# Optimization experiments

Measured on AMD Instinct MI355X. Metric: run time of the kernel, lower is better.

The kernel has to match this reference:

```python
import jax, jax.numpy as jnp
import numpy as np
from jax import lax
import math

POOL = 7
SPATIAL_SCALE = 0.125
SCORE_THRESH = 0.05
NMS_THRESH = 0.5
DET_PER_IMG = 100
NUM_CLASSES = 81
NUM_STAGES = 3
FEAT_CH = 256
CLIP_VAL = math.log(1000.0 / 16)
STDS = ((0.1, 0.1, 0.2, 0.2), (0.05, 0.05, 0.1, 0.1), (0.033, 0.033, 0.067, 0.067))


def setup_inputs() -> dict:
    key = jax.random.key(0)
    ks = jax.random.split(key, 12)
    B, N, img = 2, 512, 512
    features = jax.random.normal(ks[0], (B, FEAT_CH, 64, 64), jnp.float32)
    cx = jax.random.uniform(ks[1], (B, N)) * img
    cy = jax.random.uniform(ks[2], (B, N)) * img
    w = 16.0 + jax.random.uniform(ks[3], (B, N)) * 240.0
    h = 16.0 + jax.random.uniform(ks[4], (B, N)) * 240.0
    proposals = jnp.stack([
        jnp.clip(cx - 0.5 * w, 0.0, img), jnp.clip(cy - 0.5 * h, 0.0, img),
        jnp.clip(cx + 0.5 * w, 0.0, img), jnp.clip(cy + 0.5 * h, 0.0, img)], axis=-1)
    in_dim = FEAT_CH * POOL * POOL
    sc = 0.02
    return {
        'features': features,
        'proposals': proposals,
        'fc1_w': jax.random.normal(ks[5], (NUM_STAGES, in_dim, 1024), jnp.float32) * sc,
        'fc1_b': jnp.zeros((NUM_STAGES, 1024), jnp.float32),
        'fc2_w': jax.random.normal(ks[6], (NUM_STAGES, 1024, 1024), jnp.float32) * sc,
        'fc2_b': jnp.zeros((NUM_STAGES, 1024), jnp.float32),
        'cls_w': jax.random.normal(ks[7], (NUM_STAGES, 1024, NUM_CLASSES), jnp.float32) * sc,
        'cls_b': jnp.zeros((NUM_STAGES, NUM_CLASSES), jnp.float32),
        'bbox_w': jax.random.normal(ks[8], (NUM_STAGES, 1024, 4), jnp.float32) * sc,
        'bbox_b': jnp.zeros((NUM_STAGES, 4), jnp.float32),
        'image_size': 512,
    }


def _bilinear(feat, gx, gy):
    # feat [C,H,W]; gx,gy [N,P,P] float coords
    C, H, W = feat.shape
    x = jnp.clip(gx, 0.0, W - 1.0)
    y = jnp.clip(gy, 0.0, H - 1.0)
    x0f, y0f = jnp.floor(x), jnp.floor(y)
    x0 = x0f.astype(jnp.int32)
    y0 = y0f.astype(jnp.int32)
    x1 = jnp.minimum(x0 + 1, W - 1)
    y1 = jnp.minimum(y0 + 1, H - 1)
    dx = (x - x0f)[None]
    dy = (y - y0f)[None]
    v = (feat[:, y0, x0] * (1 - dy) * (1 - dx) + feat[:, y0, x1] * (1 - dy) * dx
         + feat[:, y1, x0] * dy * (1 - dx) + feat[:, y1, x1] * dy * dx)
    return v  # [C,N,P,P]


def roi_align(feat, boxes):
    # feat [C,H,W], boxes [N,4] in feature-map coords
    x1, y1, x2, y2 = boxes[:, 0], boxes[:, 1], boxes[:, 2], boxes[:, 3]
    bw = jnp.maximum(x2 - x1, 1.0) / POOL
    bh = jnp.maximum(y2 - y1, 1.0) / POOL
    c = jnp.arange(POOL, dtype=boxes.dtype) + 0.5
    xs = x1[:, None] + c * bw[:, None]  # [N,P]
    ys = y1[:, None] + c * bh[:, None]
    N = boxes.shape[0]
    gx = jnp.broadcast_to(xs[:, None, :], (N, POOL, POOL))
    gy = jnp.broadcast_to(ys[:, :, None], (N, POOL, POOL))
    return jnp.transpose(_bilinear(feat, gx, gy), (1, 0, 2, 3))  # [N,C,P,P]


def decode_boxes(proposals, deltas, stds):
    px1, py1, px2, py2 = proposals[:, 0], proposals[:, 1], proposals[:, 2], proposals[:, 3]
    pw = jnp.maximum(px2 - px1, 1e-6)
    ph = jnp.maximum(py2 - py1, 1e-6)
    pcx = px1 + 0.5 * pw
    pcy = py1 + 0.5 * ph
    wx, wy, ww, wh = stds
    dx = deltas[:, 0] * wx
    dy = deltas[:, 1] * wy
    dw = jnp.minimum(deltas[:, 2] * ww, CLIP_VAL)
    dh = jnp.minimum(deltas[:, 3] * wh, CLIP_VAL)
    cx = dx * pw + pcx
    cy = dy * ph + pcy
    w = jnp.exp(dw) * pw
    h = jnp.exp(dh) * ph
    return jnp.stack([cx - 0.5 * w, cy - 0.5 * h, cx + 0.5 * w, cy + 0.5 * h], axis=1)


def clip_boxes(b, img):
    return jnp.stack([jnp.clip(b[:, 0], 0.0, img), jnp.clip(b[:, 1], 0.0, img),
                      jnp.clip(b[:, 2], 0.0, img), jnp.clip(b[:, 3], 0.0, img)], axis=1)


def nms_per_image(boxes, probs, img):
    # boxes [N,4], probs [N,C]
    N, C = probs.shape
    Cm = C - 1  # skip background class 0
    labels = jnp.broadcast_to(jnp.arange(1, C, dtype=jnp.int32), (N, Cm)).reshape(-1)
    b = jnp.broadcast_to(boxes[:, None, :], (N, Cm, 4)).reshape(-1, 4)
    s = probs[:, 1:].reshape(-1)
    ws = b[:, 2] - b[:, 0]
    hs = b[:, 3] - b[:, 1]
    valid = (s > SCORE_THRESH) & (ws >= 1.0) & (hs >= 1.0)
    s = jnp.where(valid, s, -1.0)
    # class-offset trick == batched_nms
    ob = b + (labels.astype(b.dtype) * (img + 2.0))[:, None]
    area = jnp.maximum(ob[:, 2] - ob[:, 0], 0.0) * jnp.maximum(ob[:, 3] - ob[:, 1], 0.0)

    def step(s_live, _):
        i = jnp.argmax(s_live)
        si = s_live[i]
        bi = ob[i]
        ix1 = jnp.maximum(bi[0], ob[:, 0])
        iy1 = jnp.maximum(bi[1], ob[:, 1])
        ix2 = jnp.minimum(bi[2], ob[:, 2])
        iy2 = jnp.minimum(bi[3], ob[:, 3])
        inter = jnp.maximum(ix2 - ix1, 0.0) * jnp.maximum(iy2 - iy1, 0.0)
        iou = inter / (area[i] + area - inter + 1e-9)
        s_live = jnp.where(iou > NMS_THRESH, -1.0, s_live)
        s_live = s_live.at[i].set(-1.0)
        return s_live, (i, si)

    _, (idx, sel_s) = lax.scan(step, s, None, length=DET_PER_IMG)
    flag = sel_s > 0.0
    out_boxes = jnp.where(flag[:, None], b[idx], 0.0)
    out_scores = jnp.where(flag, sel_s, 0.0)
    out_labels = jnp.where(flag, labels[idx], 0)
    return out_boxes, out_scores, out_labels


def reference(features, proposals, fc1_w, fc1_b, fc2_w, fc2_b, cls_w, cls_b, bbox_w, bbox_b, image_size):
    B, Cf, H, W = features.shape
    N = proposals.shape[1]
    img = float(image_size)
    cur = proposals  # [B,N,4]
    logits = None
    for st in range(NUM_STAGES):
        pooled = jax.vmap(lambda f, bx: roi_align(f, bx * SPATIAL_SCALE))(features, cur)  # [B,N,C,P,P]
        x = pooled.reshape(B * N, -1)
        x = jax.nn.relu(x @ fc1_w[st] + fc1_b[st])
        x = jax.nn.relu(x @ fc2_w[st] + fc2_b[st])
        logits = x @ cls_w[st] + cls_b[st]  # [B*N, C]
        deltas = x @ bbox_w[st] + bbox_b[st]  # [B*N, 4]
        dec = clip_boxes(decode_boxes(cur.reshape(-1, 4), deltas, STDS[st]), img)
        cur = dec.reshape(B, N, 4)
    probs = jax.nn.softmax(logits.reshape(B, N, -1), axis=-1)
    boxes, scores, labels = jax.vmap(lambda bb, pp: nms_per_image(bb, pp, img))(cur, probs)
    return boxes, scores, labels
```

## Files before the change

### kernel.cpp

```cpp
#include <hip/hip_runtime.h>
#include <math.h>

#define NPROP 512
#define NB 2
#define NROWS (NB*NPROP)
#define FCH 256
#define FH 64
#define FW 64
#define INDIM (FCH*7*7)
#define HID 1024
#define NCLS 81
#define CAND_PER_IMG (NPROP*(NCLS-1))
#define CLIPV 4.1351666f

typedef _Float16 f16x8 __attribute__((ext_vector_type(8)));
typedef float f32x4 __attribute__((ext_vector_type(4)));
typedef unsigned int u32;
typedef unsigned long long u64;

__device__ __forceinline__ void gload16(const void* g, void* l) {
    __builtin_amdgcn_global_load_lds((const __attribute__((address_space(1))) u32*)g,
                                     (__attribute__((address_space(3))) u32*)l, 16, 0, 0);
}


#define XHI_OFF    0ull
#define XLO_OFF    25690112ull
#define WT1HI_OFF  51380224ull
#define WT1LO_OFF  77070336ull
#define WT2HI_OFF  102760448ull
#define WT2LO_OFF  104857600ull
#define H1HI_OFF   106954752ull
#define H1LO_OFF   109051904ull
#define H2_OFF     111149056ull
#define CWT_OFF    115343360ull
#define BWT_OFF    116338688ull
#define PROBS_OFF  116387840ull
#define CUR_OFF    116719616ull
#define CNT_OFF    116736000ull
#define CCS_OFF    116737024ull
#define CCOB_OFF   117064704ull
#define CCAR_OFF   118375424ull
#define CCBX_OFF   118703104ull
#define CCIX_OFF   120013824ull
#define SVS_OFF    120341504ull
#define SVB_OFF    120423424ull
#define SVI_OFF    120751104ull
#define SVC_OFF    120833024ull
#define PART_OFF   121489408ull

__global__ void init_kernel(int* ccnt) {
    if (threadIdx.x < 160) ccnt[threadIdx.x] = 0;
}

__global__ __launch_bounds__(256) void roi_align_kernel(
    const float* __restrict__ feat, const float* __restrict__ boxes,
    _Float16* __restrict__ Xhi, _Float16* __restrict__ Xlo)
{
    int r = blockIdx.x;
    int b = r >> 9;
    const float* f = feat + (size_t)b * (FCH*FH*FW);
    __shared__ float sb[4];
    __shared__ int   sx0[49], sx1[49], sy0[49], sy1[49];
    __shared__ float sw00[49], sw01[49], sw10[49], sw11[49];
    int tid = threadIdx.x;
    if (tid == 0) {
        float x1 = boxes[r*4+0]*0.125f, y1 = boxes[r*4+1]*0.125f;
        float x2 = boxes[r*4+2]*0.125f, y2 = boxes[r*4+3]*0.125f;
        sb[0] = x1; sb[1] = y1;
        sb[2] = fmaxf(x2-x1, 1.0f) / 7.0f;
        sb[3] = fmaxf(y2-y1, 1.0f) / 7.0f;
    }
    __syncthreads();
    if (tid < 49) {
        int py = tid / 7, px = tid - py*7;
        float gx = sb[0] + ((float)px + 0.5f)*sb[2];
        float gy = sb[1] + ((float)py + 0.5f)*sb[3];
        gx = fminf(fmaxf(gx, 0.0f), 63.0f);
        gy = fminf(fmaxf(gy, 0.0f), 63.0f);
        float x0f = floorf(gx), y0f = floorf(gy);
        int x0 = (int)x0f, y0 = (int)y0f;
        sx0[tid] = x0; sy0[tid] = y0;
        sx1[tid] = min(x0+1, 63); sy1[tid] = min(y0+1, 63);
        float dx = gx - x0f, dy = gy - y0f;
        sw00[tid] = (1.0f-dy)*(1.0f-dx);
        sw01[tid] = (1.0f-dy)*dx;
        sw10[tid] = dy*(1.0f-dx);
        sw11[tid] = dy*dx;
    }
    __syncthreads();
    for (int i = tid; i < INDIM; i += 256) {
        int c = i / 49;
        int p = i - c*49;
        const float* fc = f + c*(FH*FW);
        int r0 = sy0[p]*FW, r1 = sy1[p]*FW;
        float v = fc[r0 + sx0[p]]*sw00[p] + fc[r0 + sx1[p]]*sw01[p]
                + fc[r1 + sx0[p]]*sw10[p] + fc[r1 + sx1[p]]*sw11[p];
        float vs = v * 32.0f;
        _Float16 h = (_Float16)vs;
        size_t idx = ((size_t)(i >> 3) << 13) + ((size_t)r << 3) + (i & 7);
        Xhi[idx] = h;
        Xlo[idx] = (_Float16)(vs - (float)h);
    }
}

__global__ __launch_bounds__(256) void trans_limb(
    const float* __restrict__ in, _Float16* __restrict__ hi, _Float16* __restrict__ lo,
    int K, int N, float scale)
{
    __shared__ float t[32][33];
    int tx = threadIdx.x & 31, ty = threadIdx.x >> 5;
    int n0 = blockIdx.x << 5, k0 = blockIdx.y << 5;
#pragma unroll
    for (int r = 0; r < 4; ++r)
        t[ty + 8*r][tx] = in[(size_t)(k0 + ty + 8*r)*N + n0 + tx];
    __syncthreads();
#pragma unroll
    for (int r = 0; r < 4; ++r) {
        int n = n0 + ty + 8*r, k = k0 + tx;
        float v = t[tx][ty + 8*r] * scale;
        _Float16 h = (_Float16)v;
        size_t idx = ((size_t)(k >> 3)*N << 3) + ((size_t)n << 3) + (k & 7);
        hi[idx] = h;
        lo[idx] = (_Float16)(v - (float)h);
    }
}

__global__ __launch_bounds__(256) void trans_naive(
    const float* __restrict__ in, float* __restrict__ out, int K, int N, int batch)
{
    int idx = blockIdx.x*256 + threadIdx.x;
    int per = K*N;
    if (idx >= per*batch) return;
    int b = idx / per;
    int rem = idx - b*per;
    int n = rem / K, k = rem - n*K;
    out[idx] = in[(size_t)b*per + (size_t)k*N + n];
}

__global__ __launch_bounds__(512, 2) void mfma_gemm_limb256(
    const _Float16* __restrict__ Ahi, const _Float16* __restrict__ Alo,
    const _Float16* __restrict__ Bhi, const _Float16* __restrict__ Blo,
    float* __restrict__ part, int base, int extra)
{
    extern __shared__ __align__(16) char ldsraw[];
    const int tid = threadIdx.x;
    const int lane = tid & 63;
    const int w = tid >> 6;
    const int wm = w >> 2, wn = w & 3;
    const int kg = lane >> 4, lr = lane & 15;
    const int bid = blockIdx.x;
    const int z = bid & 15;
    const int tile = bid >> 4;
    const int bx = tile & 3, by = tile >> 2;
    const int row0 = by << 8, col0 = bx << 8;
    const int zsteps = base + (z < extra ? 1 : 0);
    const int o0 = ((z*base + (z < extra ? z : extra)) * 32) >> 3;

    const int sp = w >> 1;
    const int sbase = (w & 1) * 8;
    const _Float16* pl = (sp == 0) ? Ahi : (sp == 1) ? Alo : (sp == 2) ? Bhi : Blo;
    const int rc0 = (sp < 2) ? row0 : col0;
    const _Float16* sG = pl + ((size_t)(rc0 + lane) << 3);

    f32x4 acc[8][4];
#pragma unroll
    for (int i = 0; i < 8; ++i)
#pragma unroll
        for (int j = 0; j < 4; ++j) acc[i][j] = (f32x4){0.f, 0.f, 0.f, 0.f};

    auto STAGE = [&](int bufoff, int koct) {
#pragma unroll
        for (int j = 0; j < 8; ++j) {
            int sub = sbase + j;
            int ks = sub >> 2, rblk = sub & 3;
            const void* g = (const void*)(sG + ((size_t)(o0 + koct + ks) << 13)
                                             + ((size_t)rblk << 9));
            void* l = (void*)(ldsraw + bufoff + sp*16384 + ks*4096 + rblk*1024);
            gload16(g, l);
        }
    };

    STAGE(0, 0);
    if (zsteps > 1) STAGE(65536, 4);

    for (int t = 0; t < zsteps; ++t) {
        if (t + 1 < zsteps) asm volatile("s_waitcnt vmcnt(8)" ::: "memory");
        else                asm volatile("s_waitcnt vmcnt(0)" ::: "memory");
        __builtin_amdgcn_s_barrier();
        asm volatile("" ::: "memory");
        const char* Lb = ldsraw + ((t & 1) ? 65536 : 0);
        f16x8 Bh[4], Bl[4];
#pragma unroll
        for (int ni = 0; ni < 4; ++ni) {
            int s = (kg*256 + wn*64 + ni*16 + lr) * 16;
            Bh[ni] = *(const f16x8*)(Lb + 2*16384 + s);
            Bl[ni] = *(const f16x8*)(Lb + 3*16384 + s);
        }
#pragma unroll
        for (int mi = 0; mi < 8; ++mi) {
            int s = (kg*256 + wm*128 + mi*16 + lr) * 16;
            f16x8 ah = *(const f16x8*)(Lb + s);
            f16x8 al = *(const f16x8*)(Lb + 16384 + s);
#pragma unroll
            for (int ni = 0; ni < 4; ++ni) {
                acc[mi][ni] = __builtin_amdgcn_mfma_f32_16x16x32_f16(ah, Bh[ni], acc[mi][ni], 0, 0, 0);
                acc[mi][ni] = __builtin_amdgcn_mfma_f32_16x16x32_f16(ah, Bl[ni], acc[mi][ni], 0, 0, 0);
                acc[mi][ni] = __builtin_amdgcn_mfma_f32_16x16x32_f16(al, Bh[ni], acc[mi][ni], 0, 0, 0);
            }
        }
        asm volatile("" ::: "memory");
        __builtin_amdgcn_s_barrier();
        asm volatile("" ::: "memory");
        if (t + 2 < zsteps) STAGE((t & 1) ? 65536 : 0, (t+2)*4);
    }

    float* cb = part + ((size_t)z << 20)
              + (size_t)row0*HID + col0 + wn*64 + lr;
#pragma unroll
    for (int mi = 0; mi < 8; ++mi) {
#pragma unroll
        for (int j = 0; j < 4; ++j) {
            int row = wm*128 + mi*16 + kg*4 + j;
            float* pr = cb + (size_t)row*HID;
            pr[0]  = acc[mi][0][j];
            pr[16] = acc[mi][1][j];
            pr[32] = acc[mi][2][j];
            pr[48] = acc[mi][3][j];
        }
    }
}

__global__ __launch_bounds__(256) void mfma_gemm_limb(
    const _Float16* __restrict__ Ahi, const _Float16* __restrict__ Alo,
    const _Float16* __restrict__ Bhi, const _Float16* __restrict__ Blo,
    float* __restrict__ part, int base, int extra, int lognz)
{
    __shared__ __align__(16) _Float16 lds[2][4][512][8];
    const int tid = threadIdx.x;
    const int lane = tid & 63;
    const int w = tid >> 6, wm = w >> 1, wn = w & 1;
    const int kg = lane >> 4, lr = lane & 15;
    const int bid = blockIdx.x;
    const int nzm = (1 << lognz) - 1;
    const int z = bid & nzm;
    const int bx = (bid >> lognz) & 7;
    const int by = bid >> (lognz + 3);
    const int row0 = by << 7, col0 = bx << 7;
    const int zsteps = base + (z < extra ? 1 : 0);
    const int o0 = ((z*base + (z < extra ? z : extra)) * 32) >> 3;
    const int r_ = tid & 127;
    const int ks1 = tid >> 7;
    const int wb = tid & 192;

    const _Float16* srcA0 = Ahi + ((size_t)(row0 + r_) << 3);
    const _Float16* srcA1 = Alo + ((size_t)(row0 + r_) << 3);
    const _Float16* srcB0 = Bhi + ((size_t)(col0 + r_) << 3);
    const _Float16* srcB1 = Blo + ((size_t)(col0 + r_) << 3);

    f32x4 acc[4][4];
#pragma unroll
    for (int i = 0; i < 4; ++i)
#pragma unroll
        for (int j = 0; j < 4; ++j) acc[i][j] = (f32x4){0.f, 0.f, 0.f, 0.f};

#define STAGE(bf, oct) do { \
    _Float16* Lb = &lds[bf][0][0][0]; \
    gload16(srcA0 + ((size_t)(o0+(oct)+ks1  ) << 13), (void*)(Lb + (0*512 +       wb)*8)); \
    gload16(srcA0 + ((size_t)(o0+(oct)+ks1+2) << 13), (void*)(Lb + (0*512 + 256 + wb)*8)); \
    gload16(srcA1 + ((size_t)(o0+(oct)+ks1  ) << 13), (void*)(Lb + (1*512 +       wb)*8)); \
    gload16(srcA1 + ((size_t)(o0+(oct)+ks1+2) << 13), (void*)(Lb + (1*512 + 256 + wb)*8)); \
    gload16(srcB0 + ((size_t)(o0+(oct)+ks1  ) << 13), (void*)(Lb + (2*512 +       wb)*8)); \
    gload16(srcB0 + ((size_t)(o0+(oct)+ks1+2) << 13), (void*)(Lb + (2*512 + 256 + wb)*8)); \
    gload16(srcB1 + ((size_t)(o0+(oct)+ks1  ) << 13), (void*)(Lb + (3*512 +       wb)*8)); \
    gload16(srcB1 + ((size_t)(o0+(oct)+ks1+2) << 13), (void*)(Lb + (3*512 + 256 + wb)*8)); \
} while (0)

    STAGE(0, 0);
    if (1 < zsteps) STAGE(1, 4);
    for (int t = 0; t < zsteps; ++t) {
        if (t + 1 < zsteps) asm volatile("s_waitcnt vmcnt(8)" ::: "memory");
        else                asm volatile("s_waitcnt vmcnt(0)" ::: "memory");
        __builtin_amdgcn_s_barrier();
        const _Float16* Lr = &lds[t & 1][0][0][0];
        f16x8 Ah[4], Al[4], Bh[4], Bl[4];
#pragma unroll
        for (int mi = 0; mi < 4; ++mi) {
            int s = kg*128 + wm*64 + mi*16 + lr;
            Ah[mi] = *(const f16x8*)(Lr + (0*512 + s)*8);
            Al[mi] = *(const f16x8*)(Lr + (1*512 + s)*8);
        }
#pragma unroll
        for (int ni = 0; ni < 4; ++ni) {
            int s = kg*128 + wn*64 + ni*16 + lr;
            Bh[ni] = *(const f16x8*)(Lr + (2*512 + s)*8);
            Bl[ni] = *(const f16x8*)(Lr + (3*512 + s)*8);
        }
        asm volatile("s_waitcnt lgkmcnt(0)" ::: "memory");
        __builtin_amdgcn_sched_barrier(0);
        __builtin_amdgcn_s_barrier();
        if (t + 2 < zsteps) STAGE(t & 1, (t+2)*4);
#pragma unroll
        for (int mi = 0; mi < 4; ++mi)
#pragma unroll
            for (int ni = 0; ni < 4; ++ni) {
                acc[mi][ni] = __builtin_amdgcn_mfma_f32_16x16x32_f16(Ah[mi], Bh[ni], acc[mi][ni], 0, 0, 0);
                acc[mi][ni] = __builtin_amdgcn_mfma_f32_16x16x32_f16(Ah[mi], Bl[ni], acc[mi][ni], 0, 0, 0);
                acc[mi][ni] = __builtin_amdgcn_mfma_f32_16x16x32_f16(Al[mi], Bh[ni], acc[mi][ni], 0, 0, 0);
            }
    }
#undef STAGE

    float* cb = part + ((size_t)z << 20)
              + (size_t)row0*HID + col0 + wn*64 + lr;
#pragma unroll
    for (int mi = 0; mi < 4; ++mi) {
#pragma unroll
        for (int j = 0; j < 4; ++j) {
            int row = wm*64 + mi*16 + kg*4 + j;
            float* pr = cb + (size_t)row*HID;
            pr[0]  = acc[mi][0][j];
            pr[16] = acc[mi][1][j];
            pr[32] = acc[mi][2][j];
            pr[48] = acc[mi][3][j];
        }
    }
}

__global__ __launch_bounds__(256) void reduce_bias_relu(
    const float* __restrict__ part, const float* __restrict__ bias,
    float* __restrict__ out32, _Float16* __restrict__ outhi, _Float16* __restrict__ outlo,
    int nsplit, int mode)
{
    int gid = blockIdx.x*256 + threadIdx.x;
    float s = 0.f;
    for (int p = 0; p < nsplit; ++p) s += part[((size_t)p << 20) + gid];
    s = s * (1.0f/2048.0f) + bias[gid & (HID-1)];
    s = fmaxf(s, 0.f);
    if (mode == 0) {
        out32[gid] = s;
    } else {
        float vs = s * 32.0f;
        _Float16 h = (_Float16)vs;
        int row = gid >> 10, col = gid & 1023;
        size_t idx = ((size_t)(col >> 3) << 13) + ((size_t)row << 3) + (col & 7);
        outhi[idx] = h;
        outlo[idx] = (_Float16)(vs - (float)h);
    }
}

__global__ __launch_bounds__(512) void heads_kernel(
    const float* __restrict__ X, const float* __restrict__ cwT, const float* __restrict__ cb,
    const float* __restrict__ bwT, const float* __restrict__ bbb,
    float* __restrict__ cur, float* __restrict__ probs,
    const int* __restrict__ img_sz, int stage, int write_probs)
{
    __shared__ float xs[4][1024];
    __shared__ float lg[4][96];
    int tid = threadIdx.x;
    int lr = tid >> 7;
    int j  = tid & 127;
    int row0 = blockIdx.x * 4;
    for (int i = tid; i < 4096; i += 512)
        xs[i >> 10][i & 1023] = X[(size_t)(row0 + (i >> 10))*1024 + (i & 1023)];
    __syncthreads();
    int row = row0 + lr;
    if (j < 85) {
        const float* wrow = (j < 81) ? (cwT + (size_t)j*HID) : (bwT + (size_t)(j-81)*HID);
        float acc = (j < 81) ? cb[j] : bbb[j-81];
        const float4* w4 = (const float4*)wrow;
#pragma unroll 4
        for (int k4 = 0; k4 < 256; ++k4) {
            float4 wv = w4[k4];
            const float* xr = &xs[lr][k4*4];
            acc = fmaf(xr[0], wv.x, acc);
            acc = fmaf(xr[1], wv.y, acc);
            acc = fmaf(xr[2], wv.z, acc);
            acc = fmaf(xr[3], wv.w, acc);
        }
        lg[lr][j] = acc;
    }
    __syncthreads();
    if (j == 0) {
        float img = (float)(*img_sz);
        float px1 = cur[row*4+0], py1 = cur[row*4+1];
        float px2 = cur[row*4+2], py2 = cur[row*4+3];
        float pw = fmaxf(px2-px1, 1e-6f), ph = fmaxf(py2-py1, 1e-6f);
        float pcx = px1 + 0.5f*pw, pcy = py1 + 0.5f*ph;
        float wx, wy, ww, wh;
        if (stage == 0)      { wx=0.1f;   wy=0.1f;   ww=0.2f;   wh=0.2f;   }
        else if (stage == 1) { wx=0.05f;  wy=0.05f;  ww=0.1f;   wh=0.1f;   }
        else                 { wx=0.033f; wy=0.033f; ww=0.067f; wh=0.067f; }
        float dx = lg[lr][81]*wx, dy = lg[lr][82]*wy;
        float dw = fminf(lg[lr][83]*ww, CLIPV);
        float dh = fminf(lg[lr][84]*wh, CLIPV);
        float cx = dx*pw + pcx, cy = dy*ph + pcy;
        float w = expf(dw)*pw, h = expf(dh)*ph;
        cur[row*4+0] = fminf(fmaxf(cx - 0.5f*w, 0.f), img);
        cur[row*4+1] = fminf(fmaxf(cy - 0.5f*h, 0.f), img);
        cur[row*4+2] = fminf(fmaxf(cx + 0.5f*w, 0.f), img);
        cur[row*4+3] = fminf(fmaxf(cy + 0.5f*h, 0.f), img);
    }
    if (write_probs) {
        if (j == 1) {
            float m = lg[lr][0];
            for (int c2 = 1; c2 < 81; ++c2) m = fmaxf(m, lg[lr][c2]);
            float s = 0.f;
            for (int c2 = 0; c2 < 81; ++c2) s += expf(lg[lr][c2] - m);
            lg[lr][88] = m; lg[lr][89] = s;
        }
        __syncthreads();
        if (j < 81)
            probs[(size_t)row*81 + j] = expf(lg[lr][j] - lg[lr][88]) / lg[lr][89];
    }
}

__global__ __launch_bounds__(256) void compact_class(
    const float* __restrict__ probs, const float* __restrict__ cur,
    const int* __restrict__ img_sz, int* __restrict__ ccnt,
    float* __restrict__ ccs, float4* __restrict__ ccob, float* __restrict__ ccar,
    float4* __restrict__ ccbx, int* __restrict__ ccix)
{
    int gid = blockIdx.x*256 + threadIdx.x;
    if (gid >= NB*CAND_PER_IMG) return;
    int b = gid / CAND_PER_IMG;
    int rem = gid - b*CAND_PER_IMG;
    int n = rem / 80;
    int cm = rem - n*80;
    int label = cm + 1;
    int r = b*NPROP + n;
    float s = probs[(size_t)r*81 + label];
    float b0 = cur[r*4+0], b1 = cur[r*4+1], b2 = cur[r*4+2], b3 = cur[r*4+3];
    if (s > 0.05f && (b2 - b0) >= 1.0f && (b3 - b1) >= 1.0f) {
        int cls = b*80 + cm;
        int pos = atomicAdd(&ccnt[cls], 1);
        int base = cls*512 + pos;
        float img = (float)(*img_sz);
        float t = (float)label * (img + 2.0f);
        float o0 = b0+t, o1 = b1+t, o2 = b2+t, o3 = b3+t;
        ccs[base] = s;
        ccob[base] = make_float4(o0, o1, o2, o3);
        ccar[base] = fmaxf(o2-o0, 0.f) * fmaxf(o3-o1, 0.f);
        ccbx[base] = make_float4(b0, b1, b2, b3);
        ccix[base] = rem;
    }
}

__global__ __launch_bounds__(64) void class_nms(
    const int* __restrict__ ccnt, const float* __restrict__ ccs,
    const float4* __restrict__ ccob, const float* __restrict__ ccar,
    const float4* __restrict__ ccbx, const int* __restrict__ ccix,
    float* __restrict__ svs, float4* __restrict__ svb, int* __restrict__ svi,
    int* __restrict__ svc)
{
    int cls = blockIdx.x;
    int Nc = ccnt[cls];
    int base = cls*512;
    int lane = threadIdx.x;
    __shared__ float sel[5];
    float s[8]; float4 ob[8]; float a[8]; int ix[8];
    int cntl = 0;
    for (int j = lane; j < Nc; j += 64) {
        s[cntl] = ccs[base+j]; ob[cntl] = ccob[base+j];
        a[cntl] = ccar[base+j]; ix[cntl] = ccix[base+j];
        ++cntl;
    }
    int svn = 0;
    int rounds = (Nc < 100) ? Nc : 100;
    for (int it = 0; it < rounds; ++it) {
        float bs = -1.f; int bi = 0x7fffffff;
        for (int q = 0; q < cntl; ++q)
            if (s[q] > bs || (s[q] == bs && ix[q] < bi)) { bs = s[q]; bi = ix[q]; }
        for (int off = 32; off > 0; off >>= 1) {
            float os = __shfl_xor(bs, off);
            int oi = __shfl_xor(bi, off);
            if (os > bs || (os == bs && oi < bi)) { bs = os; bi = oi; }
        }
        if (bs <= 0.f) break;
        for (int q = 0; q < cntl; ++q) {
            if (s[q] == bs && ix[q] == bi) {
                sel[0] = ob[q].x; sel[1] = ob[q].y; sel[2] = ob[q].z; sel[3] = ob[q].w;
                sel[4] = a[q];
                int slot = cls*128 + svn;
                svs[slot] = bs;
                svb[slot] = ccbx[base + lane + q*64];
                svi[slot] = bi;
                s[q] = -1.f;
            }
        }
        __syncthreads();
        float bi0 = sel[0], bi1 = sel[1], bi2 = sel[2], bi3 = sel[3], ai = sel[4];
        for (int q = 0; q < cntl; ++q) {
            if (s[q] > 0.f) {
                float ix1 = fmaxf(bi0, ob[q].x), iy1 = fmaxf(bi1, ob[q].y);
                float ix2 = fminf(bi2, ob[q].z), iy2 = fminf(bi3, ob[q].w);
                float inter = fmaxf(ix2-ix1, 0.f) * fmaxf(iy2-iy1, 0.f);
                float iou = inter / (ai + a[q] - inter + 1e-9f);
                if (iou > 0.5f) s[q] = -1.f;
            }
        }
        ++svn;
        __syncthreads();
    }
    if (lane == 0) svc[cls] = svn;
}

__global__ __launch_bounds__(256) void merge_topk(
    const float* __restrict__ svs, const float4* __restrict__ svb,
    const int* __restrict__ svi, const int* __restrict__ svc,
    float* __restrict__ out)
{
    extern __shared__ char smem[];
    u64* keys = (u64*)smem;
    u32* pay  = (u32*)(smem + 65536);
    __shared__ int off[81];
    __shared__ int n2s;
    int b = blockIdx.x, tid = threadIdx.x;
    if (tid == 0) {
        int run = 0;
        for (int c = 0; c < 80; ++c) { off[c] = run; run += svc[b*80 + c]; }
        off[80] = run;
        int n2 = 256;
        while (n2 < run) n2 <<= 1;
        n2s = n2;
    }
    __syncthreads();
    int Ns = off[80], n2 = n2s;
    for (int c = 0; c < 80; ++c) {
        int n = off[c+1] - off[c];
        int srcb = (b*80 + c)*128;
        for (int k = tid; k < n; k += 256) {
            int src = srcb + k;
            keys[off[c] + k] = ((u64)__float_as_uint(svs[src]) << 32)
                             | (u64)(0xFFFFFFFFu - (u32)svi[src]);
            pay[off[c] + k] = src;
        }
    }
    for (int i = Ns + tid; i < n2; i += 256) { keys[i] = 0; pay[i] = 0; }
    __syncthreads();
    for (int k = 2; k <= n2; k <<= 1) {
        for (int j = k >> 1; j > 0; j >>= 1) {
            for (int i = tid; i < n2; i += 256) {
                int l = i ^ j;
                if (l > i) {
                    u64 a = keys[i], bb = keys[l];
                    bool dir = ((i & k) == 0);
                    if ((a < bb) == dir) {
                        keys[i] = bb; keys[l] = a;
                        u32 p = pay[i]; pay[i] = pay[l]; pay[l] = p;
                    }
                }
            }
            __syncthreads();
        }
    }
    if (tid < 100) {
        u64 kk = keys[tid];
        if (kk != 0) {
            u32 ci = 0xFFFFFFFFu - (u32)(kk & 0xFFFFFFFFull);
            float4 bx = svb[pay[tid]];
            out[b*400 + tid*4 + 0] = bx.x;
            out[b*400 + tid*4 + 1] = bx.y;
            out[b*400 + tid*4 + 2] = bx.z;
            out[b*400 + tid*4 + 3] = bx.w;
            out[800  + b*100 + tid] = __uint_as_float((u32)(kk >> 32));
            out[1000 + b*100 + tid] = (float)((ci % 80) + 1);
        } else {
            out[b*400 + tid*4 + 0] = 0.f; out[b*400 + tid*4 + 1] = 0.f;
            out[b*400 + tid*4 + 2] = 0.f; out[b*400 + tid*4 + 3] = 0.f;
            out[800  + b*100 + tid] = 0.f;
            out[1000 + b*100 + tid] = 0.f;
        }
    }
}

extern "C" void kernel_launch(void* const* d_in, const int* in_sizes, int n_in,
                              void* d_out, int out_size, void* d_ws, size_t ws_size,
                              hipStream_t stream)
{
    const float* features  = (const float*)d_in[0];
    const float* proposals = (const float*)d_in[1];
    const float* fc1_w = (const float*)d_in[2];
    const float* fc1_b = (const float*)d_in[3];
    const float* fc2_w = (const float*)d_in[4];
    const float* fc2_b = (const float*)d_in[5];
    const float* cls_w = (const float*)d_in[6];
    const float* cls_b = (const float*)d_in[7];
    const float* bbox_w = (const float*)d_in[8];
    const float* bbox_b = (const float*)d_in[9];
    const int* img_sz = (const int*)d_in[10];
    float* out = (float*)d_out;
    char* ws = (char*)d_ws;
    _Float16* xhi   = (_Float16*)(ws + XHI_OFF);
    _Float16* xlo   = (_Float16*)(ws + XLO_OFF);
    _Float16* wt1hi = (_Float16*)(ws + WT1HI_OFF);
    _Float16* wt1lo = (_Float16*)(ws + WT1LO_OFF);
    _Float16* wt2hi = (_Float16*)(ws + WT2HI_OFF);
    _Float16* wt2lo = (_Float16*)(ws + WT2LO_OFF);
    _Float16* h1hi  = (_Float16*)(ws + H1HI_OFF);
    _Float16* h1lo  = (_Float16*)(ws + H1LO_OFF);
    float*  h2     = (float*) (ws + H2_OFF);
    float*  cwT    = (float*) (ws + CWT_OFF);
    float*  bwT    = (float*) (ws + BWT_OFF);
    float*  probs  = (float*) (ws + PROBS_OFF);
    float*  cur    = (float*) (ws + CUR_OFF);
    int*    ccnt   = (int*)   (ws + CNT_OFF);
    float*  ccs    = (float*) (ws + CCS_OFF);
    float4* ccob   = (float4*)(ws + CCOB_OFF);
    float*  ccar   = (float*) (ws + CCAR_OFF);
    float4* ccbx   = (float4*)(ws + CCBX_OFF);
    int*    ccix   = (int*)   (ws + CCIX_OFF);
    float*  svs    = (float*) (ws + SVS_OFF);
    float4* svb    = (float4*)(ws + SVB_OFF);
    int*    svi    = (int*)   (ws + SVI_OFF);
    int*    svc    = (int*)   (ws + SVC_OFF);
    float*  part   = (float*) (ws + PART_OFF);

    init_kernel<<<1, 256, 0, stream>>>(ccnt);
    hipMemcpyAsync(cur, proposals, (size_t)NROWS*4*sizeof(float),
                   hipMemcpyDeviceToDevice, stream);
    trans_naive<<<(3*NCLS*HID + 255)/256, 256, 0, stream>>>(cls_w, cwT, HID, NCLS, 3);
    trans_naive<<<(3*4*HID + 255)/256, 256, 0, stream>>>(bbox_w, bwT, HID, 4, 3);

    for (int st = 0; st < 3; ++st) {
        roi_align_kernel<<<NROWS, 256, 0, stream>>>(features, cur, xhi, xlo);
        trans_limb<<<dim3(HID/32, INDIM/32), 256, 0, stream>>>(
            fc1_w + (size_t)st*INDIM*HID, wt1hi, wt1lo, INDIM, HID, 64.0f);
        mfma_gemm_limb256<<<256, 512, 131072, stream>>>(
            xhi, xlo, wt1hi, wt1lo, part, 24, 8);
        reduce_bias_relu<<<(NROWS*HID)/256, 256, 0, stream>>>(
            part, fc1_b + st*HID, nullptr, h1hi, h1lo, 16, 1);
        trans_limb<<<dim3(HID/32, HID/32), 256, 0, stream>>>(
            fc2_w + (size_t)st*HID*HID, wt2hi, wt2lo, HID, HID, 64.0f);
        mfma_gemm_limb<<<512, 256, 0, stream>>>(
            h1hi, h1lo, wt2hi, wt2lo, part, 4, 0, 3);
        reduce_bias_relu<<<(NROWS*HID)/256, 256, 0, stream>>>(
            part, fc2_b + st*HID, h2, nullptr, nullptr, 8, 0);
        heads_kernel<<<NROWS/4, 512, 0, stream>>>(
            h2, cwT + (size_t)st*NCLS*HID, cls_b + st*NCLS,
            bwT + (size_t)st*4*HID, bbox_b + st*4,
            cur, probs, img_sz, st, st == 2 ? 1 : 0);
    }
    compact_class<<<(NB*CAND_PER_IMG)/256, 256, 0, stream>>>(
        probs, cur, img_sz, ccnt, ccs, ccob, ccar, ccbx, ccix);
    class_nms<<<160, 64, 0, stream>>>(
        ccnt, ccs, ccob, ccar, ccbx, ccix, svs, svb, svi, svc);
    merge_topk<<<NB, 256, 98304, stream>>>(
        svs, svb, svi, svc, out);
}
```

Baseline: 781.2 us.

## Stage ROI-align and weight-limb outputs in shared memory for vectorized 16-byte stores

ROI-align now handles four ROIs per block, one wavefront each. It precomputes the flat bilinear indices and weights, stages the fp16 hi/lo results in shared memory by channel chunk, and writes them out as 16-byte vectors in the k-octet-major layout instead of scattered 2-byte stores. trans_limb likewise packs eight k values per thread and issues f16x8 stores. The GEMM loop adds an explicit LDS waitcnt and a sched_barrier before the s_barrier, presumably for correctness or scheduling. The cost is more LDS use and fewer, larger ROI blocks.

```diff
diff --git a/kernel.cpp b/kernel.cpp
--- a/kernel.cpp
+++ b/kernel.cpp
@@ -12,6 +12,7 @@
 #define NCLS 81
 #define CAND_PER_IMG (NPROP*(NCLS-1))
 #define CLIPV 4.1351666f
+#define RCHUNK 1792
 
 typedef _Float16 f16x8 __attribute__((ext_vector_type(8)));
 typedef float f32x4 __attribute__((ext_vector_type(4)));
@@ -57,50 +58,63 @@
     const float* __restrict__ feat, const float* __restrict__ boxes,
     _Float16* __restrict__ Xhi, _Float16* __restrict__ Xlo)
 {
-    int r = blockIdx.x;
-    int b = r >> 9;
+    __shared__ __align__(16) _Float16 bufh[4][1800], bufl[4][1800];
+    __shared__ int   sidx[4][4][49];
+    __shared__ float swt[4][4][49];
+    const int tid = threadIdx.x;
+    const int w = tid >> 6, lane = tid & 63;
+    const int r0 = blockIdx.x << 2;
+    const int r = r0 + w;
+    const int b = r >> 9;
     const float* f = feat + (size_t)b * (FCH*FH*FW);
-    __shared__ float sb[4];
-    __shared__ int   sx0[49], sx1[49], sy0[49], sy1[49];
-    __shared__ float sw00[49], sw01[49], sw10[49], sw11[49];
-    int tid = threadIdx.x;
-    if (tid == 0) {
+
+    if (lane < 49) {
         float x1 = boxes[r*4+0]*0.125f, y1 = boxes[r*4+1]*0.125f;
         float x2 = boxes[r*4+2]*0.125f, y2 = boxes[r*4+3]*0.125f;
-        sb[0] = x1; sb[1] = y1;
-        sb[2] = fmaxf(x2-x1, 1.0f) / 7.0f;
-        sb[3] = fmaxf(y2-y1, 1.0f) / 7.0f;
-    }
-    __syncthreads();
-    if (tid < 49) {
-        int py = tid / 7, px = tid - py*7;
-        float gx = sb[0] + ((float)px + 0.5f)*sb[2];
-        float gy = sb[1] + ((float)py + 0.5f)*sb[3];
+        float bw = fmaxf(x2-x1, 1.0f) / 7.0f;
+        float bh = fmaxf(y2-y1, 1.0f) / 7.0f;
+        int py = lane / 7, px = lane - py*7;
+        float gx = x1 + ((float)px + 0.5f)*bw;
+        float gy = y1 + ((float)py + 0.5f)*bh;
         gx = fminf(fmaxf(gx, 0.0f), 63.0f);
         gy = fminf(fmaxf(gy, 0.0f), 63.0f);
         float x0f = floorf(gx), y0f = floorf(gy);
         int x0 = (int)x0f, y0 = (int)y0f;
-        sx0[tid] = x0; sy0[tid] = y0;
-        sx1[tid] = min(x0+1, 63); sy1[tid] = min(y0+1, 63);
+        int x1c = min(x0+1, 63), y1c = min(y0+1, 63);
         float dx = gx - x0f, dy = gy - y0f;
-        sw00[tid] = (1.0f-dy)*(1.0f-dx);
-        sw01[tid] = (1.0f-dy)*dx;
-        sw10[tid] = dy*(1.0f-dx);
-        sw11[tid] = dy*dx;
+        sidx[w][0][lane] = y0*FW + x0;
+        sidx[w][1][lane] = y0*FW + x1c;
+        sidx[w][2][lane] = y1c*FW + x0;
+        sidx[w][3][lane] = y1c*FW + x1c;
+        swt[w][0][lane] = (1.0f-dy)*(1.0f-dx);
+        swt[w][1][lane] = (1.0f-dy)*dx;
+        swt[w][2][lane] = dy*(1.0f-dx);
+        swt[w][3][lane] = dy*dx;
     }
     __syncthreads();
-    for (int i = tid; i < INDIM; i += 256) {
-        int c = i / 49;
-        int p = i - c*49;
-        const float* fc = f + c*(FH*FW);
-        int r0 = sy0[p]*FW, r1 = sy1[p]*FW;
-        float v = fc[r0 + sx0[p]]*sw00[p] + fc[r0 + sx1[p]]*sw01[p]
-                + fc[r1 + sx0[p]]*sw10[p] + fc[r1 + sx1[p]]*sw11[p];
-        float vs = v * 32.0f;
-        _Float16 h = (_Float16)vs;
-        size_t idx = ((size_t)(i >> 3) << 13) + ((size_t)r << 3) + (i & 7);
-        Xhi[idx] = h;
-        Xlo[idx] = (_Float16)(vs - (float)h);
+    for (int ch = 0; ch < 7; ++ch) {
+        for (int i2 = lane; i2 < RCHUNK; i2 += 64) {
+            int i = ch*RCHUNK + i2;
+            int c = i / 49;
+            int p = i - c*49;
+            const float* fc = f + c*(FH*FW);
+            float v = fc[sidx[w][0][p]]*swt[w][0][p] + fc[sidx[w][1][p]]*swt[w][1][p]
+                    + fc[sidx[w][2][p]]*swt[w][2][p] + fc[sidx[w][3][p]]*swt[w][3][p];
+            float vs = v * 32.0f;
+            _Float16 h = (_Float16)vs;
+            bufh[w][i2] = h;
+            bufl[w][i2] = (_Float16)(vs - (float)h);
+        }
+        __syncthreads();
+        for (int q = tid; q < 224*4; q += 256) {
+            int oct = q >> 2, p = q & 3;
+            f16x8 hv = *(const f16x8*)&bufh[p][oct*8];
+            f16x8 lv = *(const f16x8*)&bufl[p][oct*8];
+            size_t idx = ((size_t)(ch*224 + oct) << 13) + ((size_t)(r0 + p) << 3);
+            *(f16x8*)(Xhi + idx) = hv;
+            *(f16x8*)(Xlo + idx) = lv;
+        }
+        __syncthreads();
     }
 }
 
@@ -115,14 +129,19 @@
     for (int r = 0; r < 4; ++r)
         t[ty + 8*r][tx] = in[(size_t)(k0 + ty + 8*r)*N + n0 + tx];
     __syncthreads();
-#pragma unroll
-    for (int r = 0; r < 4; ++r) {
-        int n = n0 + ty + 8*r, k = k0 + tx;
-        float v = t[tx][ty + 8*r] * scale;
-        _Float16 h = (_Float16)v;
-        size_t idx = ((size_t)(k >> 3)*N << 3) + ((size_t)n << 3) + (k & 7);
-        hi[idx] = h;
-        lo[idx] = (_Float16)(v - (float)h);
+    if (ty < 4) {
+        int n = n0 + tx;
+        f16x8 hv, lv;
+#pragma unroll
+        for (int e = 0; e < 8; ++e) {
+            float v = t[ty*8 + e][tx] * scale;
+            _Float16 h = (_Float16)v;
+            hv[e] = h;
+            lv[e] = (_Float16)(v - (float)h);
+        }
+        size_t idx = (((size_t)(k0 >> 3) + ty)*N << 3) + ((size_t)n << 3);
+        *(f16x8*)(hi + idx) = hv;
+        *(f16x8*)(lo + idx) = lv;
     }
 }
 
@@ -209,7 +228,8 @@
                 acc[mi][ni] = __builtin_amdgcn_mfma_f32_16x16x32_f16(al, Bh[ni], acc[mi][ni], 0, 0, 0);
             }
         }
-        asm volatile("" ::: "memory");
+        asm volatile("s_waitcnt lgkmcnt(0)" ::: "memory");
+        __builtin_amdgcn_sched_barrier(0);
         __builtin_amdgcn_s_barrier();
         asm volatile("" ::: "memory");
         if (t + 2 < zsteps) STAGE((t & 1) ? 65536 : 0, (t+2)*4);
@@ -623,7 +643,7 @@
     trans_naive<<<(3*4*HID + 255)/256, 256, 0, stream>>>(bbox_w, bwT, HID, 4, 3);
 
     for (int st = 0; st < 3; ++st) {
-        roi_align_kernel<<<NROWS, 256, 0, stream>>>(features, cur, xhi, xlo);
+        roi_align_kernel<<<NROWS/4, 256, 0, stream>>>(features, cur, xhi, xlo);
         trans_limb<<<dim3(HID/32, INDIM/32), 256, 0, stream>>>(
             fc1_w + (size_t)st*INDIM*HID, wt1hi, wt1lo, INDIM, HID, 64.0f);
         mfma_gemm_limb256<<<256, 512, 131072, stream>>>(
```

New measurement: 739.2 us. 1.06x faster.
